# Performance work log

Hardware: AMD Instinct MI355X
Metric: run time of the kernel (lower is better)

## Reference

```python
import jax, jax.numpy as jnp
import numpy as np

B, N, D = 32, 1024, 128


def setup_inputs() -> dict:
    key = jax.random.key(0)
    ks = jax.random.split(key, 8)
    scale = 0.05
    P = jax.random.normal(ks[0], (B, N, D), dtype=jnp.float32)
    w_itr_att = jax.random.normal(ks[1], (3 * D,), dtype=jnp.float32) * scale
    w1 = jax.random.normal(ks[2], (2 * D, D), dtype=jnp.float32) * scale
    w2 = jax.random.normal(ks[3], (2 * D, D), dtype=jnp.float32) * scale
    w3 = jax.random.normal(ks[4], (2 * D, D), dtype=jnp.float32) * scale
    b1 = jnp.zeros((D,), dtype=jnp.float32)
    b2 = jnp.zeros((D,), dtype=jnp.float32)
    b3 = jnp.zeros((D,), dtype=jnp.float32)
    return {"P": P, "w_itr_att": w_itr_att, "w1": w1, "w2": w2,
            "w3": w3, "b1": b1, "b2": b2, "b3": b3}


def reference(P, w_itr_att, w1, w2, w3, b1, b2, b3):
    # P: [b, n, d]
    d = P.shape[-1]
    # Original builds alphaP[b,i,:,j] = concat(P[b,j], P[b,i], P[b,j]*P[b,i])
    # and A[b,i,j] = w_itr_att . alphaP[b,i,:,j]. Decompose w to avoid the
    # O(n^2 * 3d) tensor while computing identical math.
    wa, wb, wc = w_itr_att[:d], w_itr_att[d:2 * d], w_itr_att[2 * d:]
    A = (P @ wb)[:, :, None] + (P @ wa)[:, None, :] \
        + jnp.einsum('bid,bjd->bij', P * wc, P)  # [b, n, n]
    SA = jax.nn.softmax(A, axis=-1)              # softmax over j (axis=2)
    itr_attn = jnp.einsum('bij,bjd->bid', SA, P)  # batch_dot(SA, P)
    # Fuse gate (dropout is identity at inference)
    P_concat = jnp.concatenate([P, itr_attn], axis=2)  # [b, n, 2d]
    z = jnp.tanh(P_concat @ w1 + b1)
    r = jax.nn.sigmoid(P_concat @ w2 + b2)
    f = jax.nn.sigmoid(P_concat @ w3 + b3)
    return r * P + f * z
```

## Files before the change

### kernel.cpp

```cpp
#include <hip/hip_runtime.h>
#include <math.h>

#define BB 32
#define NN 1024
#define DD 128

typedef __bf16 bf16;
typedef bf16 bf16x4 __attribute__((ext_vector_type(4)));
typedef bf16 bf16x8 __attribute__((ext_vector_type(8)));
typedef float f32x4 __attribute__((ext_vector_type(4)));
typedef float f32x16 __attribute__((ext_vector_type(16)));

#define MFMA16(a, b, c) __builtin_amdgcn_mfma_f32_16x16x32_bf16(a, b, c, 0, 0, 0)
#define MFMA32(a, b, c) __builtin_amdgcn_mfma_f32_32x32x16_bf16(a, b, c, 0, 0, 0)

__device__ inline bf16x4 swap32(bf16x4 v) {
    union { bf16x4 h; int i[2]; } u, r;
    u.h = v;
    r.i[0] = __shfl_xor(u.i[0], 32, 64);
    r.i[1] = __shfl_xor(u.i[1], 32, 64);
    return r.h;
}

#define LTS 133
__global__ __launch_bounds__(256) void k_prep(const float* __restrict__ P,
                                              const float* __restrict__ w_itr,
                                              bf16* __restrict__ Xbf,
                                              bf16* __restrict__ Pq,
                                              bf16* __restrict__ Ptp,
                                              float* __restrict__ t) {
    __shared__ float Lt[64 * LTS];
    int tid = threadIdx.x;
    int b = blockIdx.x >> 4, g = blockIdx.x & 15;
    int n0 = g * 64;
    long base = ((long)b * NN + n0) * DD;
#pragma unroll
    for (int i = 0; i < 8; ++i) {
        int idx = tid + i * 256;
        int row = idx >> 5, c4 = idx & 31;
        *(float4*)&Lt[row * LTS + c4 * 4] = *(const float4*)&P[base + row * 128 + c4 * 4];
    }
    __syncthreads();
    {
        int row = tid >> 2, q = tid & 3;
        float s = 0.f;
#pragma unroll
        for (int kk = 0; kk < 32; ++kk) {
            int k = 4 * kk + q;
            s += Lt[row * LTS + k] * w_itr[k];
        }
        s += __shfl_xor(s, 1);
        s += __shfl_xor(s, 2);
        if (q == 0) t[(long)b * NN + n0 + row] = s;
    }
    const float* wc = w_itr + 2 * DD;
#pragma unroll
    for (int i = 0; i < 4; ++i) {
        int idx = tid + i * 256;
        int row = idx >> 4, seg = idx & 15;
        float4 va = *(const float4*)&Lt[row * LTS + seg * 8];
        float4 vb = *(const float4*)&Lt[row * LTS + seg * 8 + 4];
        float4 wa4 = *(const float4*)&wc[seg * 8];
        float4 wb4 = *(const float4*)&wc[seg * 8 + 4];
        float fv[8] = {va.x, va.y, va.z, va.w, vb.x, vb.y, vb.z, vb.w};
        float wv[8] = {wa4.x, wa4.y, wa4.z, wa4.w, wb4.x, wb4.y, wb4.z, wb4.w};
        bf16x8 xv, qv;
#pragma unroll
        for (int e = 0; e < 8; ++e) {
            xv[e] = (bf16)fv[e];
            qv[e] = (bf16)(fv[e] * wv[e]);
        }
        long rowg = (long)b * NN + n0 + row;
        *(bf16x8*)&Xbf[rowg * 128 + seg * 8] = xv;
        *(bf16x8*)&Pq[rowg * 128 + seg * 8] = qv;
    }
#pragma unroll
    for (int i = 0; i < 4; ++i) {
        int idx = tid + i * 256;
        int d = idx >> 3, c = idx & 7;
        bf16x8 v;
#pragma unroll
        for (int e = 0; e < 8; ++e) v[e] = (bf16)Lt[(c * 8 + e) * LTS + d];
        *(bf16x8*)&Ptp[((long)b * DD + d) * NN + n0 + c * 8] = v;
    }
}

__global__ __launch_bounds__(256) void k_prepw(const float* __restrict__ w1,
                                               const float* __restrict__ w2,
                                               const float* __restrict__ w3,
                                               bf16* __restrict__ WtG) {
    __shared__ float Lw[32][33];
    int bi = blockIdx.x;
    int mat = bi >> 5, rem = bi & 31;
    int kt = rem >> 2, ct = rem & 3;
    const float* wsrc = (mat == 0) ? w1 : ((mat == 1) ? w2 : w3);
    int tid = threadIdx.x;
#pragma unroll
    for (int p = 0; p < 4; ++p) {
        int idx = tid + p * 256;
        int kr = idx >> 5, c = idx & 31;
        Lw[kr][c] = wsrc[(kt * 32 + kr) * DD + ct * 32 + c];
    }
    __syncthreads();
    int colg = tid >> 3, kq = tid & 7;
    bf16x4 v;
#pragma unroll
    for (int e = 0; e < 4; ++e) v[e] = (bf16)Lw[kq * 4 + e][colg];
    *(bf16x4*)&WtG[(mat * 128 + ct * 32 + colg) * 256 + kt * 32 + kq * 4] = v;
}

__global__ __launch_bounds__(256, 2) void k_attn(const bf16* __restrict__ Xbf,
                                                 const bf16* __restrict__ Pq,
                                                 const bf16* __restrict__ Ptp,
                                                 const float* __restrict__ t,
                                                 const bf16* __restrict__ WtG,
                                                 const float* __restrict__ P,
                                                 const float* __restrict__ b1,
                                                 const float* __restrict__ b2,
                                                 const float* __restrict__ b3,
                                                 float* __restrict__ out) {
    __shared__ __align__(16) char smem[72704];
    bf16* Kt = (bf16*)smem;
    bf16* Vt = (bf16*)(smem + 34816);
    float* tsh = (float*)(smem + 71680);
    float* lbuf = (float*)(smem + 72192);
    float* Obuf = (float*)smem;
    bf16* Xsh = (bf16*)(smem + 34816);

    const int tid = threadIdx.x;
    const int w = tid >> 6, lane = tid & 63;
    const int col = lane & 31, q = lane >> 5;
    const int kh = w >> 1, rg = w & 1;
    const int b = blockIdx.x & 31, qt = blockIdx.x >> 5;
    const long qrow0 = (long)b * NN + qt * 64;
    const long qbase = qrow0 + rg * 32;

    bf16x8 Qb[8];
#pragma unroll
    for (int c = 0; c < 8; ++c)
        Qb[c] = *(const bf16x8*)&Pq[(qbase + col) * 128 + c * 16 + q * 8];

    f32x16 O[4];
#pragma unroll
    for (int mt = 0; mt < 4; ++mt)
#pragma unroll
        for (int r = 0; r < 16; ++r) O[mt][r] = 0.f;
    float lsum = 0.f;

    float4 kr[8], vr[8];
    float tr = 0.f;
    auto loadKV = [&](int jt) {
#pragma unroll
        for (int i = 0; i < 8; ++i) {
            int idx = tid + i * 256;
            int h = idx >> 10, rem = idx & 1023;
            kr[i] = *(const float4*)&Xbf[((long)b * NN + h * 512 + jt * 64 + (rem >> 4)) * 128 +
                                         (rem & 15) * 8];
            vr[i] = *(const float4*)&Ptp[((long)b * DD + (rem >> 3)) * NN + h * 512 + jt * 64 +
                                         (rem & 7) * 8];
        }
        tr = (tid < 128) ? t[(long)b * NN + (tid >> 6) * 512 + jt * 64 + (tid & 63)] : 0.f;
    };

    loadKV(0);
    for (int jt = 0; jt < 8; ++jt) {
        __syncthreads();
#pragma unroll
        for (int i = 0; i < 8; ++i) {
            int idx = tid + i * 256;
            int h = idx >> 10, rem = idx & 1023;
            *(float4*)&Kt[h * (64 * 136) + (rem >> 4) * 136 + (rem & 15) * 8] = kr[i];
            *(float4*)&Vt[h * (128 * 72) + (rem >> 3) * 72 + (rem & 7) * 8] = vr[i];
        }
        if (tid < 128) tsh[tid] = tr;
        __syncthreads();
        if (jt < 7) loadKV(jt + 1);

        const bf16* KtH = Kt + kh * (64 * 136);
        const bf16* VtH = Vt + kh * (128 * 72);
        const float* tH = tsh + kh * 64;
#pragma unroll
        for (int kt = 0; kt < 2; ++kt) {
            f32x16 S;
#pragma unroll
            for (int r = 0; r < 16; ++r) S[r] = 0.f;
#pragma unroll
            for (int c = 0; c < 8; ++c)
                S = MFMA32(*(const bf16x8*)&KtH[(kt * 32 + col) * 136 + c * 16 + q * 8],
                           Qb[c], S);
            float tqs[16];
#pragma unroll
            for (int i = 0; i < 4; ++i) {
                float4 tv = *(const float4*)&tH[kt * 32 + 8 * i + 4 * q];
                tqs[4 * i + 0] = tv.x; tqs[4 * i + 1] = tv.y;
                tqs[4 * i + 2] = tv.z; tqs[4 * i + 3] = tv.w;
            }
            float pv[16];
#pragma unroll
            for (int r = 0; r < 16; ++r) {
                float e = __expf(fminf(S[r] + tqs[r], 80.f));
                pv[r] = e;
                lsum += e;
            }
            bf16x4 Qd[4];
#pragma unroll
            for (int i = 0; i < 4; ++i)
#pragma unroll
                for (int e = 0; e < 4; ++e) Qd[i][e] = (bf16)pv[4 * i + e];
            bf16x4 sA = q ? Qd[0] : Qd[1];
            bf16x4 rA = swap32(sA);
            bf16x4 sB = q ? Qd[2] : Qd[3];
            bf16x4 rB = swap32(sB);
            bf16x4 lo0 = q ? rA : Qd[0], hi0 = q ? Qd[1] : rA;
            bf16x4 lo1 = q ? rB : Qd[2], hi1 = q ? Qd[3] : rB;
            bf16x8 f0, f1;
#pragma unroll
            for (int e = 0; e < 4; ++e) {
                f0[e] = lo0[e]; f0[4 + e] = hi0[e];
                f1[e] = lo1[e]; f1[4 + e] = hi1[e];
            }
#pragma unroll
            for (int mt = 0; mt < 4; ++mt) {
                O[mt] = MFMA32(*(const bf16x8*)&VtH[(mt * 32 + col) * 72 + kt * 32 + q * 8],
                               f0, O[mt]);
                O[mt] = MFMA32(*(const bf16x8*)&VtH[(mt * 32 + col) * 72 + kt * 32 + 16 + q * 8],
                               f1, O[mt]);
            }
        }
    }

    float l2 = lsum + __shfl_xor(lsum, 32, 64);
    if (q == 0) lbuf[(kh * 2 + rg) * 32 + col] = l2;
    __syncthreads();
    if (kh == 1) {
#pragma unroll
        for (int mt = 0; mt < 4; ++mt)
#pragma unroll
            for (int r = 0; r < 16; ++r) {
                int d = mt * 32 + (r & 3) + 8 * (r >> 2) + 4 * q;
                Obuf[(rg * 128 + d) * 33 + col] = O[mt][r];
            }
    } else {
        int tl = tid;
#pragma unroll
        for (int i = 0; i < 8; ++i) {
            int idx = tl + i * 128;
            int row = idx >> 4, seg = idx & 15;
            *(bf16x8*)&Xsh[row * 264 + seg * 8] =
                *(const bf16x8*)&Xbf[(qrow0 + row) * 128 + seg * 8];
        }
    }
    __syncthreads();
    if (kh == 0) {
        float linv = 1.f / (lbuf[(0 * 2 + rg) * 32 + col] + lbuf[(1 * 2 + rg) * 32 + col]);
#pragma unroll
        for (int mt = 0; mt < 4; ++mt)
#pragma unroll
            for (int r = 0; r < 16; ++r) {
                int d = mt * 32 + (r & 3) + 8 * (r >> 2) + 4 * q;
                float v = (O[mt][r] + Obuf[(rg * 128 + d) * 33 + col]) * linv;
                Xsh[(rg * 32 + col) * 264 + 128 + d] = (bf16)v;
            }
    }
    __syncthreads();

    const int ln = lane & 15, q3 = lane >> 4;
    const int ch = w >> 1, rg2 = w & 1;
    f32x4 stz[2][4], str[2][4];
#pragma unroll
    for (int mat = 0; mat < 3; ++mat) {
        f32x4 acc[2][4];
#pragma unroll
        for (int mt = 0; mt < 2; ++mt)
#pragma unroll
            for (int nt = 0; nt < 4; ++nt) acc[mt][nt] = (f32x4){0.f, 0.f, 0.f, 0.f};
#pragma unroll
        for (int kc = 0; kc < 8; ++kc) {
            bf16x8 Af0 = *(const bf16x8*)&Xsh[(rg2 * 32 + ln) * 264 + kc * 32 + q3 * 8];
            bf16x8 Af1 = *(const bf16x8*)&Xsh[(rg2 * 32 + 16 + ln) * 264 + kc * 32 + q3 * 8];
#pragma unroll
            for (int nt = 0; nt < 4; ++nt) {
                bf16x8 Bf = *(const bf16x8*)&WtG[(mat * 128 + ch * 64 + nt * 16 + ln) * 256 +
                                                 kc * 32 + q3 * 8];
                acc[0][nt] = MFMA16(Af0, Bf, acc[0][nt]);
                acc[1][nt] = MFMA16(Af1, Bf, acc[1][nt]);
            }
        }
        const float* bp = (mat == 0) ? b1 : ((mat == 1) ? b2 : b3);
#pragma unroll
        for (int mt = 0; mt < 2; ++mt)
#pragma unroll
            for (int nt = 0; nt < 4; ++nt) {
                int colc = ch * 64 + nt * 16 + ln;
                float bb = bp[colc];
#pragma unroll
                for (int r = 0; r < 4; ++r) {
                    float y = acc[mt][nt][r] + bb;
                    if (mat == 0) stz[mt][nt][r] = tanhf(y);
                    else if (mat == 1) str[mt][nt][r] = 1.f / (1.f + __expf(-y));
                    else {
                        float fg = 1.f / (1.f + __expf(-y));
                        long row = qrow0 + rg2 * 32 + mt * 16 + q3 * 4 + r;
                        float p = P[row * DD + colc];
                        out[row * DD + colc] = str[mt][nt][r] * p + fg * stz[mt][nt][r];
                    }
                }
            }
    }
}

extern "C" void kernel_launch(void* const* d_in, const int* in_sizes, int n_in,
                              void* d_out, int out_size, void* d_ws, size_t ws_size,
                              hipStream_t stream) {
    const float* P     = (const float*)d_in[0];
    const float* w_itr = (const float*)d_in[1];
    const float* w1    = (const float*)d_in[2];
    const float* w2    = (const float*)d_in[3];
    const float* w3    = (const float*)d_in[4];
    const float* b1    = (const float*)d_in[5];
    const float* b2    = (const float*)d_in[6];
    const float* b3    = (const float*)d_in[7];
    float* out = (float*)d_out;

    char* wsb = (char*)d_ws;
    bf16* Xbf  = (bf16*)(wsb);
    bf16* Pq   = (bf16*)(wsb + 8388608);
    bf16* Ptp  = (bf16*)(wsb + 16777216);
    float* tws = (float*)(wsb + 25165824);
    bf16* WtG  = (bf16*)(wsb + 25296896);

    k_prep<<<dim3(BB * 16), dim3(256), 0, stream>>>(P, w_itr, Xbf, Pq, Ptp, tws);
    k_prepw<<<dim3(96), dim3(256), 0, stream>>>(w1, w2, w3, WtG);
    k_attn<<<dim3(512), dim3(256), 0, stream>>>(Xbf, Pq, Ptp, tws, WtG, P, b1, b2, b3, out);
}
```

Baseline: 198.0 us.

## Shrink shared memory and registers to fit three blocks per CU

The attention loop now stages one 64-key tile per iteration in place of two halves at once, looping 16 times instead of 8. This halves the K/V staging buffers and the prefetch registers. The cross-wave O reduction goes through shared memory in bf16. The gate GEMM stages weight tiles in shared memory and gives each wave 16 rows by 128 columns. The final residual reads P from the bf16 copy in shared memory instead of fp32 global. Launch bounds rise to 3 blocks per CU for more occupancy, at the cost of more barriers and bf16 rounding of the partial O and the residual P.

Result: no change. 200.6 us (+1.3%).

```diff
diff --git a/kernel.cpp b/kernel.cpp
--- a/kernel.cpp
+++ b/kernel.cpp
@@ -109,23 +109,23 @@
     *(bf16x4*)&WtG[(mat * 128 + ct * 32 + colg) * 256 + kt * 32 + kq * 4] = v;
 }
 
-__global__ __launch_bounds__(256, 2) void k_attn(const bf16* __restrict__ Xbf,
+__global__ __launch_bounds__(256, 3) void k_attn(const bf16* __restrict__ Xbf,
                                                  const bf16* __restrict__ Pq,
                                                  const bf16* __restrict__ Ptp,
                                                  const float* __restrict__ t,
                                                  const bf16* __restrict__ WtG,
-                                                 const float* __restrict__ P,
                                                  const float* __restrict__ b1,
                                                  const float* __restrict__ b2,
                                                  const float* __restrict__ b3,
                                                  float* __restrict__ out) {
-    __shared__ __align__(16) char smem[72704];
+    __shared__ __align__(16) char smem[52736];
     bf16* Kt = (bf16*)smem;
-    bf16* Vt = (bf16*)(smem + 34816);
-    float* tsh = (float*)(smem + 71680);
-    float* lbuf = (float*)(smem + 72192);
-    float* Obuf = (float*)smem;
-    bf16* Xsh = (bf16*)(smem + 34816);
+    bf16* Vt = (bf16*)(smem + 17408);
+    float* tsh = (float*)(smem + 35840);
+    float* lbuf = (float*)(smem + 52224);
+    bf16* Xsh = (bf16*)smem;
+    bf16* Obf = (bf16*)(smem + 33792);
+    bf16* Wst = (bf16*)(smem + 33792);
 
     const int tid = threadIdx.x;
     const int w = tid >> 6, lane = tid & 63;
@@ -147,85 +147,80 @@
         for (int r = 0; r < 16; ++r) O[mt][r] = 0.f;
     float lsum = 0.f;
 
-    float4 kr[8], vr[8];
+    float4 kr[4], vr[4];
     float tr = 0.f;
     auto loadKV = [&](int jt) {
-#pragma unroll
-        for (int i = 0; i < 8; ++i) {
+        int j0 = jt * 64;
+#pragma unroll
+        for (int i = 0; i < 4; ++i) {
             int idx = tid + i * 256;
-            int h = idx >> 10, rem = idx & 1023;
-            kr[i] = *(const float4*)&Xbf[((long)b * NN + h * 512 + jt * 64 + (rem >> 4)) * 128 +
-                                         (rem & 15) * 8];
-            vr[i] = *(const float4*)&Ptp[((long)b * DD + (rem >> 3)) * NN + h * 512 + jt * 64 +
-                                         (rem & 7) * 8];
-        }
-        tr = (tid < 128) ? t[(long)b * NN + (tid >> 6) * 512 + jt * 64 + (tid & 63)] : 0.f;
+            kr[i] = *(const float4*)&Xbf[((long)b * NN + j0 + (idx >> 4)) * 128 +
+                                         (idx & 15) * 8];
+            vr[i] = *(const float4*)&Ptp[((long)b * DD + (idx >> 3)) * NN + j0 +
+                                         (idx & 7) * 8];
+        }
+        tr = (tid < 64) ? t[(long)b * NN + j0 + tid] : 0.f;
     };
 
     loadKV(0);
-    for (int jt = 0; jt < 8; ++jt) {
+    for (int jt = 0; jt < 16; ++jt) {
         __syncthreads();
 #pragma unroll
-        for (int i = 0; i < 8; ++i) {
+        for (int i = 0; i < 4; ++i) {
             int idx = tid + i * 256;
-            int h = idx >> 10, rem = idx & 1023;
-            *(float4*)&Kt[h * (64 * 136) + (rem >> 4) * 136 + (rem & 15) * 8] = kr[i];
-            *(float4*)&Vt[h * (128 * 72) + (rem >> 3) * 72 + (rem & 7) * 8] = vr[i];
-        }
-        if (tid < 128) tsh[tid] = tr;
+            *(float4*)&Kt[(idx >> 4) * 136 + (idx & 15) * 8] = kr[i];
+            *(float4*)&Vt[(idx >> 3) * 72 + (idx & 7) * 8] = vr[i];
+        }
+        if (tid < 64) tsh[tid] = tr;
         __syncthreads();
-        if (jt < 7) loadKV(jt + 1);
-
-        const bf16* KtH = Kt + kh * (64 * 136);
-        const bf16* VtH = Vt + kh * (128 * 72);
-        const float* tH = tsh + kh * 64;
-#pragma unroll
-        for (int kt = 0; kt < 2; ++kt) {
-            f32x16 S;
-#pragma unroll
-            for (int r = 0; r < 16; ++r) S[r] = 0.f;
-#pragma unroll
-            for (int c = 0; c < 8; ++c)
-                S = MFMA32(*(const bf16x8*)&KtH[(kt * 32 + col) * 136 + c * 16 + q * 8],
-                           Qb[c], S);
-            float tqs[16];
-#pragma unroll
-            for (int i = 0; i < 4; ++i) {
-                float4 tv = *(const float4*)&tH[kt * 32 + 8 * i + 4 * q];
-                tqs[4 * i + 0] = tv.x; tqs[4 * i + 1] = tv.y;
-                tqs[4 * i + 2] = tv.z; tqs[4 * i + 3] = tv.w;
-            }
-            float pv[16];
-#pragma unroll
-            for (int r = 0; r < 16; ++r) {
-                float e = __expf(fminf(S[r] + tqs[r], 80.f));
-                pv[r] = e;
-                lsum += e;
-            }
-            bf16x4 Qd[4];
-#pragma unroll
-            for (int i = 0; i < 4; ++i)
-#pragma unroll
-                for (int e = 0; e < 4; ++e) Qd[i][e] = (bf16)pv[4 * i + e];
-            bf16x4 sA = q ? Qd[0] : Qd[1];
-            bf16x4 rA = swap32(sA);
-            bf16x4 sB = q ? Qd[2] : Qd[3];
-            bf16x4 rB = swap32(sB);
-            bf16x4 lo0 = q ? rA : Qd[0], hi0 = q ? Qd[1] : rA;
-            bf16x4 lo1 = q ? rB : Qd[2], hi1 = q ? Qd[3] : rB;
-            bf16x8 f0, f1;
-#pragma unroll
-            for (int e = 0; e < 4; ++e) {
-                f0[e] = lo0[e]; f0[4 + e] = hi0[e];
-                f1[e] = lo1[e]; f1[4 + e] = hi1[e];
-            }
-#pragma unroll
-            for (int mt = 0; mt < 4; ++mt) {
-                O[mt] = MFMA32(*(const bf16x8*)&VtH[(mt * 32 + col) * 72 + kt * 32 + q * 8],
-                               f0, O[mt]);
-                O[mt] = MFMA32(*(const bf16x8*)&VtH[(mt * 32 + col) * 72 + kt * 32 + 16 + q * 8],
-                               f1, O[mt]);
-            }
+        if (jt < 15) loadKV(jt + 1);
+
+        const bf16* KtH = Kt + kh * 32 * 136;
+        const float* tH = tsh + kh * 32;
+
+        f32x16 S;
+#pragma unroll
+        for (int r = 0; r < 16; ++r) S[r] = 0.f;
+#pragma unroll
+        for (int c = 0; c < 8; ++c)
+            S = MFMA32(*(const bf16x8*)&KtH[col * 136 + c * 16 + q * 8], Qb[c], S);
+        float tqs[16];
+#pragma unroll
+        for (int i = 0; i < 4; ++i) {
+            float4 tv = *(const float4*)&tH[8 * i + 4 * q];
+            tqs[4 * i + 0] = tv.x; tqs[4 * i + 1] = tv.y;
+            tqs[4 * i + 2] = tv.z; tqs[4 * i + 3] = tv.w;
+        }
+        float pv[16];
+#pragma unroll
+        for (int r = 0; r < 16; ++r) {
+            float e = __expf(fminf(S[r] + tqs[r], 80.f));
+            pv[r] = e;
+            lsum += e;
+        }
+        bf16x4 Qd[4];
+#pragma unroll
+        for (int i = 0; i < 4; ++i)
+#pragma unroll
+            for (int e = 0; e < 4; ++e) Qd[i][e] = (bf16)pv[4 * i + e];
+        bf16x4 sA = q ? Qd[0] : Qd[1];
+        bf16x4 rA = swap32(sA);
+        bf16x4 sB = q ? Qd[2] : Qd[3];
+        bf16x4 rB = swap32(sB);
+        bf16x4 lo0 = q ? rA : Qd[0], hi0 = q ? Qd[1] : rA;
+        bf16x4 lo1 = q ? rB : Qd[2], hi1 = q ? Qd[3] : rB;
+        bf16x8 f0, f1;
+#pragma unroll
+        for (int e = 0; e < 4; ++e) {
+            f0[e] = lo0[e]; f0[4 + e] = hi0[e];
+            f1[e] = lo1[e]; f1[4 + e] = hi1[e];
+        }
+#pragma unroll
+        for (int mt = 0; mt < 4; ++mt) {
+            O[mt] = MFMA32(*(const bf16x8*)&Vt[(mt * 32 + col) * 72 + kh * 32 + q * 8],
+                           f0, O[mt]);
+            O[mt] = MFMA32(*(const bf16x8*)&Vt[(mt * 32 + col) * 72 + kh * 32 + 16 + q * 8],
+                           f1, O[mt]);
         }
     }
 
@@ -238,13 +233,12 @@
 #pragma unroll
             for (int r = 0; r < 16; ++r) {
                 int d = mt * 32 + (r & 3) + 8 * (r >> 2) + 4 * q;
-                Obuf[(rg * 128 + d) * 33 + col] = O[mt][r];
+                Obf[(rg * 128 + d) * 36 + col] = (bf16)O[mt][r];
             }
     } else {
-        int tl = tid;
 #pragma unroll
         for (int i = 0; i < 8; ++i) {
-            int idx = tl + i * 128;
+            int idx = tid + i * 128;
             int row = idx >> 4, seg = idx & 15;
             *(bf16x8*)&Xsh[row * 264 + seg * 8] =
                 *(const bf16x8*)&Xbf[(qrow0 + row) * 128 + seg * 8];
@@ -252,60 +246,64 @@
     }
     __syncthreads();
     if (kh == 0) {
-        float linv = 1.f / (lbuf[(0 * 2 + rg) * 32 + col] + lbuf[(1 * 2 + rg) * 32 + col]);
+        float linv = 1.f / (lbuf[rg * 32 + col] + lbuf[(2 + rg) * 32 + col]);
 #pragma unroll
         for (int mt = 0; mt < 4; ++mt)
 #pragma unroll
             for (int r = 0; r < 16; ++r) {
                 int d = mt * 32 + (r & 3) + 8 * (r >> 2) + 4 * q;
-                float v = (O[mt][r] + Obuf[(rg * 128 + d) * 33 + col]) * linv;
+                float v = (O[mt][r] + (float)Obf[(rg * 128 + d) * 36 + col]) * linv;
                 Xsh[(rg * 32 + col) * 264 + 128 + d] = (bf16)v;
             }
     }
-    __syncthreads();
 
     const int ln = lane & 15, q3 = lane >> 4;
-    const int ch = w >> 1, rg2 = w & 1;
-    f32x4 stz[2][4], str[2][4];
+    f32x4 gz[8], gr[8];
 #pragma unroll
     for (int mat = 0; mat < 3; ++mat) {
-        f32x4 acc[2][4];
-#pragma unroll
-        for (int mt = 0; mt < 2; ++mt)
-#pragma unroll
-            for (int nt = 0; nt < 4; ++nt) acc[mt][nt] = (f32x4){0.f, 0.f, 0.f, 0.f};
-#pragma unroll
-        for (int kc = 0; kc < 8; ++kc) {
-            bf16x8 Af0 = *(const bf16x8*)&Xsh[(rg2 * 32 + ln) * 264 + kc * 32 + q3 * 8];
-            bf16x8 Af1 = *(const bf16x8*)&Xsh[(rg2 * 32 + 16 + ln) * 264 + kc * 32 + q3 * 8];
-#pragma unroll
-            for (int nt = 0; nt < 4; ++nt) {
-                bf16x8 Bf = *(const bf16x8*)&WtG[(mat * 128 + ch * 64 + nt * 16 + ln) * 256 +
-                                                 kc * 32 + q3 * 8];
-                acc[0][nt] = MFMA16(Af0, Bf, acc[0][nt]);
-                acc[1][nt] = MFMA16(Af1, Bf, acc[1][nt]);
+        f32x4 acc[8];
+#pragma unroll
+        for (int nt = 0; nt < 8; ++nt) acc[nt] = (f32x4){0.f, 0.f, 0.f, 0.f};
+#pragma unroll
+        for (int k2 = 0; k2 < 4; ++k2) {
+            __syncthreads();
+#pragma unroll
+            for (int i = 0; i < 4; ++i) {
+                int idx = tid + i * 256;
+                *(float4*)&Wst[(idx >> 3) * 72 + (idx & 7) * 8] =
+                    *(const float4*)&WtG[(mat * 128 + (idx >> 3)) * 256 + k2 * 64 +
+                                         (idx & 7) * 8];
+            }
+            __syncthreads();
+#pragma unroll
+            for (int kc2 = 0; kc2 < 2; ++kc2) {
+                bf16x8 Af = *(const bf16x8*)&Xsh[(w * 16 + ln) * 264 + k2 * 64 +
+                                                 kc2 * 32 + q3 * 8];
+#pragma unroll
+                for (int nt = 0; nt < 8; ++nt) {
+                    bf16x8 Bf = *(const bf16x8*)&Wst[(nt * 16 + ln) * 72 + kc2 * 32 + q3 * 8];
+                    acc[nt] = MFMA16(Af, Bf, acc[nt]);
+                }
             }
         }
         const float* bp = (mat == 0) ? b1 : ((mat == 1) ? b2 : b3);
 #pragma unroll
-        for (int mt = 0; mt < 2; ++mt)
-#pragma unroll
-            for (int nt = 0; nt < 4; ++nt) {
-                int colc = ch * 64 + nt * 16 + ln;
-                float bb = bp[colc];
-#pragma unroll
-                for (int r = 0; r < 4; ++r) {
-                    float y = acc[mt][nt][r] + bb;
-                    if (mat == 0) stz[mt][nt][r] = tanhf(y);
-                    else if (mat == 1) str[mt][nt][r] = 1.f / (1.f + __expf(-y));
-                    else {
-                        float fg = 1.f / (1.f + __expf(-y));
-                        long row = qrow0 + rg2 * 32 + mt * 16 + q3 * 4 + r;
-                        float p = P[row * DD + colc];
-                        out[row * DD + colc] = str[mt][nt][r] * p + fg * stz[mt][nt][r];
-                    }
+        for (int nt = 0; nt < 8; ++nt) {
+            int colc = nt * 16 + ln;
+            float bb = bp[colc];
+#pragma unroll
+            for (int r = 0; r < 4; ++r) {
+                float y = acc[nt][r] + bb;
+                if (mat == 0) gz[nt][r] = tanhf(y);
+                else if (mat == 1) gr[nt][r] = 1.f / (1.f + __expf(-y));
+                else {
+                    float fg = 1.f / (1.f + __expf(-y));
+                    int lrow = w * 16 + q3 * 4 + r;
+                    float p = (float)Xsh[lrow * 264 + colc];
+                    out[(qrow0 + lrow) * 128 + colc] = gr[nt][r] * p + fg * gz[nt][r];
                 }
             }
+        }
     }
 }
 
@@ -331,5 +329,5 @@
 
     k_prep<<<dim3(BB * 16), dim3(256), 0, stream>>>(P, w_itr, Xbf, Pq, Ptp, tws);
     k_prepw<<<dim3(96), dim3(256), 0, stream>>>(w1, w2, w3, WtG);
-    k_attn<<<dim3(512), dim3(256), 0, stream>>>(Xbf, Pq, Ptp, tws, WtG, P, b1, b2, b3, out);
-}
+    k_attn<<<dim3(512), dim3(256), 0, stream>>>(Xbf, Pq, Ptp, tws, WtG, b1, b2, b3, out);
+}
```
